# Kernel tuning notes

Hardware: AMD Instinct MI355X
Metric: run time of the kernel (lower is better)

## Reference

```python
import jax, jax.numpy as jnp
import numpy as np
import math

EMBED = 1024
HEADS = 16
HEAD_DIM = EMBED // HEADS


def setup_inputs() -> dict:
    key = jax.random.key(0)
    ks = jax.random.split(key, 9)
    B, S = 2, 2048
    query = jax.random.normal(ks[0], (B, S, EMBED), dtype=jnp.float32)
    key_t = jax.random.normal(ks[1], (B, S, EMBED), dtype=jnp.float32)
    value = jax.random.normal(ks[2], (B, S, EMBED), dtype=jnp.float32)
    mask = jax.random.randint(ks[3], (B, 1, S, S), 0, 2, dtype=jnp.int32)
    # nn.Linear(head_dim, head_dim, bias=False) weights: [out, in]
    sc = 1.0 / math.sqrt(HEAD_DIM)
    Wq = jax.random.uniform(ks[4], (HEAD_DIM, HEAD_DIM), jnp.float32, -sc, sc)
    Wk = jax.random.uniform(ks[5], (HEAD_DIM, HEAD_DIM), jnp.float32, -sc, sc)
    Wv = jax.random.uniform(ks[6], (HEAD_DIM, HEAD_DIM), jnp.float32, -sc, sc)
    so = 1.0 / math.sqrt(EMBED)
    Wo = jax.random.uniform(ks[7], (EMBED, EMBED), jnp.float32, -so, so)
    bo = jax.random.uniform(ks[8], (EMBED,), jnp.float32, -so, so)
    return {"query": query, "key": key_t, "value": value, "mask": mask,
            "Wq": Wq, "Wk": Wk, "Wv": Wv, "Wo": Wo, "bo": bo}


def reference(query, key, value, mask, Wq, Wk, Wv, Wo, bo):
    B, Sq, E = query.shape
    Sk = key.shape[1]
    H, D = HEADS, HEAD_DIM
    # Faithful raw reshape into heads (as in the torch source, no transpose)
    q = query.reshape(B, H, Sq, D)
    k = key.reshape(B, H, Sk, D)
    v = value.reshape(B, H, Sk, D)
    # per-head_dim Linear (bias-free): x @ W.T
    Q = jnp.einsum('bhsd,ed->bhse', q, Wq)
    K = jnp.einsum('bhsd,ed->bhse', k, Wk)
    V = jnp.einsum('bhsd,ed->bhse', v, Wv)
    scores = jnp.einsum('bhqd,bhkd->bhqk', Q, K)  # [B,H,Sq,Sk]
    scores = jnp.where(mask == 0, jnp.float32(-1e20), scores)
    # NOTE: source divides by sqrt(embed_size), not sqrt(head_dim)
    attn = jax.nn.softmax(scores / jnp.float32(math.sqrt(E)), axis=-1)
    out = jnp.einsum('bhqk,bhkd->bhqd', attn, V).reshape(B, Sq, H * D)
    return out @ Wo.T + bo
```

## Files before the change

### kernel.cpp

```cpp
#include <hip/hip_runtime.h>

typedef __attribute__((ext_vector_type(8))) short short8;
typedef __attribute__((ext_vector_type(4))) float f32x4;
typedef __attribute__((ext_vector_type(2))) int int2v;
typedef __attribute__((ext_vector_type(4))) int int4v;

__device__ __forceinline__ short f2bf(float f) {
  unsigned u = __builtin_bit_cast(unsigned, f);
  u += 0x7fff + ((u >> 16) & 1);
  return (short)(u >> 16);
}

__device__ __forceinline__ int pk2bf(float lo, float hi) {
#if defined(__gfx950__) && __has_builtin(__builtin_amdgcn_cvt_pk_bf16_f32)
  typedef __attribute__((ext_vector_type(2))) __bf16 bf16x2;
  bf16x2 v = __builtin_amdgcn_cvt_pk_bf16_f32(lo, hi);
  return __builtin_bit_cast(int, v);
#else
  return (int)(unsigned short)(short)f2bf(lo) | (((int)f2bf(hi)) << 16);
#endif
}

__device__ __forceinline__ short8 pack8(f32x4 a, f32x4 b) {
  int4v t;
  t.x = pk2bf(a[0], a[1]);
  t.y = pk2bf(a[2], a[3]);
  t.z = pk2bf(b[0], b[1]);
  t.w = pk2bf(b[2], b[3]);
  return __builtin_bit_cast(short8, t);
}

__device__ __forceinline__ float fand(float p, int m) {
  return __builtin_bit_cast(float, __builtin_bit_cast(int, p) & m);
}

__device__ __forceinline__ float fexp2(float x) {
#if __has_builtin(__builtin_amdgcn_exp2f)
  return __builtin_amdgcn_exp2f(x);
#else
  return exp2f(x);
#endif
}

__device__ __forceinline__ float bf2f(short s) {
  return __builtin_bit_cast(float, ((int)(unsigned short)s) << 16);
}

__device__ __forceinline__ void glds16(const short* g, short* lbase, int lane) {
#if __has_builtin(__builtin_amdgcn_global_load_lds)
  __builtin_amdgcn_global_load_lds(
      (const __attribute__((address_space(1))) unsigned int*)g,
      (__attribute__((address_space(3))) unsigned int*)lbase, 16, 0, 0);
#else
  *(short8*)(lbase + lane * 8) = *(const short8*)g;
#endif
}

__global__ __launch_bounds__(256) void prep(const float* __restrict__ q,
                                            const float* __restrict__ k,
                                            const float* __restrict__ v,
                                            const float* __restrict__ Wq,
                                            const float* __restrict__ Wk,
                                            const float* __restrict__ Wv,
                                            const float* __restrict__ Wo,
                                            const int* __restrict__ mask,
                                            short* __restrict__ Qp,
                                            short* __restrict__ Kp,
                                            short* __restrict__ Vtp,
                                            short* __restrict__ Wob,
                                            unsigned* __restrict__ mmod) {
  const int bid = blockIdx.x;
  const int tid = threadIdx.x;

  if (bid >= 4096) {
    const int mb = bid - 4096;
    const int ka = mb & 31, bq = mb >> 5;
    const int b_ = bq >> 4, qb = bq & 15;
    const int wv = tid >> 6, qd = (tid >> 4) & 3, m16_ = tid & 15;
    const int* mbase = mask + b_ * 4194304 + (qb * 128 + wv * 32) * 2048 + ka * 64 + m16_;
    unsigned d = 0;
#pragma unroll
    for (int p = 0; p < 8; ++p) {
      const int* mr = mbase + ((p >> 2) * 16 + qd * 4 + (p & 3)) * 2048;
#pragma unroll
      for (int bb = 0; bb < 4; ++bb)
        if (mr[bb * 16] != 0) d |= 1u << (p * 4 + bb);
    }
    mmod[mb * 256 + tid] = d;
    return;
  }
  if (bid >= 3072) {
    const int i = ((bid - 3072) * 256 + tid) * 4;
    const f32x4 x = *(const f32x4*)&Wo[i];
    int2v o;
    o.x = pk2bf(x[0], x[1]);
    o.y = pk2bf(x[2], x[3]);
    *(int2v*)&Wob[i] = o;
    return;
  }

  __shared__ short xt[64][72];
  __shared__ short ot[64][72];
  const int mode = bid >> 10;
  const int bt = bid & 1023;
  const float* X;
  const float* W;
  float scale;
  if (mode == 0) { X = q; W = Wq; scale = 0.045084220f; }
  else if (mode == 1) { X = k; W = Wk; scale = 1.0f; }
  else { X = v; W = Wv; scale = 1.0f; }

  const int r0 = bt * 64;
  const int row = tid >> 2, seg = (tid & 3) * 16;
  const f32x4* xs = (const f32x4*)(X + (r0 + row) * 64 + seg);
  const f32x4 x0 = xs[0], x1 = xs[1], x2 = xs[2], x3 = xs[3];
  *(short8*)&xt[row][seg] = pack8(x0, x1);
  *(short8*)&xt[row][seg + 8] = pack8(x2, x3);
  __syncthreads();

  const int lane = tid & 63, wave = tid >> 6;
  const int m16 = lane & 15, quad = lane >> 4;

  const short8 a0 = *(const short8*)&xt[wave * 16 + m16][quad * 8];
  const short8 a1 = *(const short8*)&xt[wave * 16 + m16][32 + quad * 8];

  f32x4 acc[4];
#pragma unroll
  for (int nt = 0; nt < 4; ++nt) {
    const f32x4* wp0 = (const f32x4*)&W[(nt * 16 + m16) * 64 + quad * 8];
    const f32x4* wp1 = (const f32x4*)&W[(nt * 16 + m16) * 64 + 32 + quad * 8];
    const short8 b0 = pack8(wp0[0], wp0[1]);
    const short8 b1 = pack8(wp1[0], wp1[1]);
    f32x4 z = (f32x4){0.f, 0.f, 0.f, 0.f};
    z = __builtin_amdgcn_mfma_f32_16x16x32_bf16(a0, b0, z, 0, 0, 0);
    z = __builtin_amdgcn_mfma_f32_16x16x32_bf16(a1, b1, z, 0, 0, 0);
    acc[nt] = z;
  }

  if (mode != 2) {
#pragma unroll
    for (int nt = 0; nt < 4; ++nt)
#pragma unroll
      for (int r = 0; r < 4; ++r)
        ot[wave * 16 + quad * 4 + r][nt * 16 + m16] = f2bf(acc[nt][r] * scale);
  } else {
#pragma unroll
    for (int nt = 0; nt < 4; ++nt)
#pragma unroll
      for (int r = 0; r < 4; ++r)
        ot[nt * 16 + m16][16 * quad + 4 * r + wave] = f2bf(acc[nt][r]);
  }
  __syncthreads();

  const int orow = tid >> 2, opart = tid & 3;
  if (mode != 2) {
    short* dst = (mode == 0 ? Qp : Kp) + (r0 + orow) * 64 + opart * 16;
    *(short8*)&dst[0] = *(const short8*)&ot[orow][opart * 16];
    *(short8*)&dst[8] = *(const short8*)&ot[orow][opart * 16 + 8];
  } else {
    const int bh = r0 >> 11, s0 = r0 & 2047;
    short* dst = Vtp + bh * 131072 + orow * 2048 + s0 + opart * 16;
    *(short8*)&dst[0] = *(const short8*)&ot[orow][opart * 16];
    *(short8*)&dst[8] = *(const short8*)&ot[orow][opart * 16 + 8];
  }
}

__global__ __launch_bounds__(256) void flashs(const short* __restrict__ Qp,
                                              const short* __restrict__ Kp,
                                              const short* __restrict__ Vt,
                                              const unsigned* __restrict__ mmod,
                                              short* __restrict__ Opart,
                                              float* __restrict__ lpart) {
  __shared__ __attribute__((aligned(16))) short kt[2][4096];
  __shared__ __attribute__((aligned(16))) short vt[2][4096];
  __shared__ __attribute__((aligned(16))) short pt[128][72];
  const int tid = threadIdx.x;
  const int bid = blockIdx.x;
  const int local = bid >> 3;
  const int khalf = local & 1;
  const int qblk = (local >> 1) & 15;
  const int bh = (bid & 7) * 4 + (local >> 5);
  const int q0 = qblk << 7;
  const int b = bh >> 4;
  const short* Qh = Qp + bh * 131072;
  const short* Kh = Kp + bh * 131072;
  const short* Vh = Vt + bh * 131072;
  const int lane = tid & 63, wave = tid >> 6;
  const int m16 = lane & 15, quad = lane >> 4;
  const int srow = lane >> 3, sj = (lane & 7) ^ srow;
  const int msh = m16 * 4;
  const int koff = m16 * 128 + ((quad ^ (m16 & 7)) * 16);
  const unsigned* mqb = mmod + (b * 16 + qblk) * 32 * 256 + tid;

  short8 aq[2][2];
#pragma unroll
  for (int g = 0; g < 2; ++g)
#pragma unroll
    for (int h = 0; h < 2; ++h)
      aq[g][h] = *(const short8*)&Qh[(q0 + wave * 32 + g * 16 + m16) * 64 + h * 32 + quad * 8];

  float l[2][4];
  f32x4 oacc[2][4];
#pragma unroll
  for (int g = 0; g < 2; ++g)
#pragma unroll
    for (int r = 0; r < 4; ++r) l[g][r] = 0.f;
#pragma unroll
  for (int g = 0; g < 2; ++g)
#pragma unroll
    for (int dt = 0; dt < 4; ++dt) oacc[g][dt] = (f32x4){0.f, 0.f, 0.f, 0.f};

  const int kaEnd = khalf * 16 + 15;

  auto stage = [&](int buf, int ka) {
#pragma unroll
    for (int t = 0; t < 2; ++t) {
      const int crow = wave * 16 + t * 8;
      glds16(Kh + (ka * 64 + crow + srow) * 64 + sj * 8, &kt[buf][crow * 64], lane);
      glds16(Vh + (crow + srow) * 2048 + ka * 64 + sj * 8, &vt[buf][crow * 64], lane);
    }
  };

  auto body = [&](int ka, int buf, unsigned mwU, unsigned& mwN) {
    __syncthreads();
    if (ka < kaEnd) {
      stage(buf ^ 1, ka + 1);
      mwN = mqb[(ka + 1) * 256];
    }

    f32x4 s[2][4];
#pragma unroll
    for (int nt = 0; nt < 4; ++nt) {
      const int o0 = nt * 2048 + koff;
      const short8 kb0 = *(const short8*)((const char*)&kt[buf][0] + o0);
      const short8 kb1 = *(const short8*)((const char*)&kt[buf][0] + (o0 ^ 64));
#pragma unroll
      for (int g = 0; g < 2; ++g) {
        f32x4 z = (f32x4){0.f, 0.f, 0.f, 0.f};
        z = __builtin_amdgcn_mfma_f32_16x16x32_bf16(aq[g][0], kb0, z, 0, 0, 0);
        z = __builtin_amdgcn_mfma_f32_16x16x32_bf16(aq[g][1], kb1, z, 0, 0, 0);
        s[g][nt] = z;
      }
    }

#pragma unroll
    for (int g = 0; g < 2; ++g) {
#pragma unroll
      for (int r = 0; r < 4; ++r) {
        const int pb = (g * 4 + r) * 4;
        float p[4];
#pragma unroll
        for (int nt = 0; nt < 4; ++nt) {
          const int m = ((int)(mwU << (31 - (pb + nt)))) >> 31;
          p[nt] = fand(fexp2(s[g][nt][r]), m);
        }
        l[g][r] += (p[0] + p[1]) + (p[2] + p[3]);
        int2v pp;
        pp.x = pk2bf(p[0], p[1]);
        pp.y = pk2bf(p[2], p[3]);
        *(int2v*)&pt[wave * 32 + g * 16 + quad * 4 + r][msh] = pp;
      }
    }

    short8 ap[2][2];
#pragma unroll
    for (int g = 0; g < 2; ++g)
#pragma unroll
      for (int h = 0; h < 2; ++h)
        ap[g][h] = *(const short8*)&pt[wave * 32 + g * 16 + m16][h * 32 + quad * 8];

#pragma unroll
    for (int dt = 0; dt < 4; ++dt) {
      const int o0 = dt * 2048 + koff;
      const short8 vb0 = *(const short8*)((const char*)&vt[buf][0] + o0);
      const short8 vb1 = *(const short8*)((const char*)&vt[buf][0] + (o0 ^ 64));
#pragma unroll
      for (int g = 0; g < 2; ++g) {
        f32x4 z = oacc[g][dt];
        z = __builtin_amdgcn_mfma_f32_16x16x32_bf16(ap[g][0], vb0, z, 0, 0, 0);
        z = __builtin_amdgcn_mfma_f32_16x16x32_bf16(ap[g][1], vb1, z, 0, 0, 0);
        oacc[g][dt] = z;
      }
    }
  };

  unsigned mwA, mwB = 0;
  const int ka0 = khalf * 16;
  stage(0, ka0);
  mwA = mqb[ka0 * 256];

  for (int kk = 0; kk < 8; ++kk) {
    body(ka0 + 2 * kk, 0, mwA, mwB);
    body(ka0 + 2 * kk + 1, 1, mwB, mwA);
  }

  short* Oh = Opart + khalf * 4194304;
  float* lh = lpart + khalf * 65536;
#pragma unroll
  for (int g = 0; g < 2; ++g)
#pragma unroll
    for (int r = 0; r < 4; ++r) {
#pragma unroll
      for (int off = 1; off < 16; off <<= 1) l[g][r] += __shfl_xor(l[g][r], off, 16);
      const float inv = 1.0f / l[g][r];
#pragma unroll
      for (int dt = 0; dt < 4; ++dt)
        pt[wave * 32 + g * 16 + quad * 4 + r][dt * 16 + m16] = f2bf(oacc[g][dt][r] * inv);
      if (m16 == 0) lh[bh * 2048 + q0 + wave * 32 + g * 16 + quad * 4 + r] = l[g][r];
    }

  const int orow = lane >> 1, opart = lane & 1;
  const int prow = wave * 32 + orow;
  short* og = Oh + (bh * 2048 + q0 + prow) * 64 + opart * 32;
#pragma unroll
  for (int c = 0; c < 32; c += 8)
    *(short8*)&og[c] = *(const short8*)&pt[prow][opart * 32 + c];
}

__global__ __launch_bounds__(256) void combineO(const short* __restrict__ O0,
                                                const short* __restrict__ O1,
                                                const float* __restrict__ lp,
                                                short* __restrict__ Ob) {
  const int gid = blockIdx.x * 256 + threadIdx.x;
  const int e0 = gid * 8;
  const int row = e0 >> 6;
  const float l1 = lp[row], l2 = lp[65536 + row];
  const float is = 1.0f / (l1 + l2);
  const float w1 = l1 * is, w2 = l2 * is;
  const short8 a = *(const short8*)&O0[e0];
  const short8 c = *(const short8*)&O1[e0];
  float f[8];
#pragma unroll
  for (int j = 0; j < 8; ++j) f[j] = w1 * bf2f(a[j]) + w2 * bf2f(c[j]);
  int4v o;
  o.x = pk2bf(f[0], f[1]);
  o.y = pk2bf(f[2], f[3]);
  o.z = pk2bf(f[4], f[5]);
  o.w = pk2bf(f[6], f[7]);
  *(short8*)&Ob[e0] = __builtin_bit_cast(short8, o);
}

__global__ __launch_bounds__(256) void outproj(const short* __restrict__ Ob,
                                               const short* __restrict__ Wob,
                                               const float* __restrict__ bo,
                                               float* __restrict__ out) {
  __shared__ short at[64][72];
  __shared__ short bt[128][72];
  const int tid = threadIdx.x;
  const int bid = blockIdx.x;
  const int ct = bid >> 6, rt = bid & 63;
  const int r0 = rt * 64, c0 = ct * 128;
  const int lane = tid & 63, wave = tid >> 6;
  const int mr = (wave >> 1) * 32, nc = (wave & 1) * 64;
  const int m16 = lane & 15, quad = lane >> 4;
  const int arow = tid >> 2, apart = tid & 3;
  const int brow = tid >> 1, bhalf = (tid & 1) * 32;

  f32x4 acc[2][4];
#pragma unroll
  for (int mt = 0; mt < 2; ++mt)
#pragma unroll
    for (int nt = 0; nt < 4; ++nt) acc[mt][nt] = (f32x4){0.f, 0.f, 0.f, 0.f};

  for (int kc = 0; kc < 16; ++kc) {
    __syncthreads();
    const short* ag = &Ob[(r0 + arow) * 1024 + kc * 64 + apart * 16];
    const short* bg = &Wob[(c0 + brow) * 1024 + kc * 64 + bhalf];
    *(short8*)&at[arow][apart * 16] = *(const short8*)&ag[0];
    *(short8*)&at[arow][apart * 16 + 8] = *(const short8*)&ag[8];
    *(short8*)&bt[brow][bhalf] = *(const short8*)&bg[0];
    *(short8*)&bt[brow][bhalf + 8] = *(const short8*)&bg[8];
    *(short8*)&bt[brow][bhalf + 16] = *(const short8*)&bg[16];
    *(short8*)&bt[brow][bhalf + 24] = *(const short8*)&bg[24];
    __syncthreads();

#pragma unroll
    for (int kh = 0; kh < 2; ++kh) {
      short8 af[2], bf[4];
#pragma unroll
      for (int i = 0; i < 2; ++i)
        af[i] = *(const short8*)&at[mr + i * 16 + m16][kh * 32 + quad * 8];
#pragma unroll
      for (int j = 0; j < 4; ++j)
        bf[j] = *(const short8*)&bt[nc + j * 16 + m16][kh * 32 + quad * 8];
#pragma unroll
      for (int mt = 0; mt < 2; ++mt)
#pragma unroll
        for (int nt = 0; nt < 4; ++nt)
          acc[mt][nt] = __builtin_amdgcn_mfma_f32_16x16x32_bf16(af[mt], bf[nt], acc[mt][nt], 0, 0, 0);
    }
  }

#pragma unroll
  for (int nt = 0; nt < 4; ++nt) {
    const int col = c0 + nc + nt * 16 + m16;
    const float bias = bo[col];
#pragma unroll
    for (int mt = 0; mt < 2; ++mt)
#pragma unroll
      for (int rr = 0; rr < 4; ++rr)
        out[(r0 + mr + mt * 16 + quad * 4 + rr) * 1024 + col] = acc[mt][nt][rr] + bias;
  }
}

extern "C" void kernel_launch(void* const* d_in, const int* in_sizes, int n_in,
                              void* d_out, int out_size, void* d_ws, size_t ws_size,
                              hipStream_t stream) {
  const float* query = (const float*)d_in[0];
  const float* key = (const float*)d_in[1];
  const float* value = (const float*)d_in[2];
  const int* mask = (const int*)d_in[3];
  const float* Wq = (const float*)d_in[4];
  const float* Wk = (const float*)d_in[5];
  const float* Wv = (const float*)d_in[6];
  const float* Wo = (const float*)d_in[7];
  const float* bo = (const float*)d_in[8];
  float* out = (float*)d_out;

  char* ws = (char*)d_ws;
  short* Qp = (short*)(ws);
  short* Kp = (short*)(ws + 8388608);
  short* Vt = (short*)(ws + 16777216);
  short* Opart = (short*)(ws + 25165824);
  short* Wob = (short*)(ws + 41943040);
  float* lp = (float*)(ws + 44040192);
  unsigned* mmod = (unsigned*)(ws + 44564480);
  short* Ob = Qp;

  prep<<<5120, 256, 0, stream>>>(query, key, value, Wq, Wk, Wv, Wo, mask,
                                 Qp, Kp, Vt, Wob, mmod);
  flashs<<<1024, 256, 0, stream>>>(Qp, Kp, Vt, mmod, Opart, lp);
  combineO<<<2048, 256, 0, stream>>>(Opart, Opart + 4194304, lp, Ob);
  outproj<<<512, 256, 0, stream>>>(Ob, Wob, bo, out);
}
```

Baseline: 246.3 us.

## Drop LDS staging in flash kernel, shrink q-tile, fuse split-K combine into outproj

The attention kernel now reads K and V fragments straight from global memory instead of double-buffering them through LDS with async loads. It uses 64-query tiles (one 16-row group per wave), doubling the grid to 2048 blocks, and declares occupancy 4 in launch bounds. The mask bit layout is regenerated to match the new tile shape. The combineO kernel is removed: the output projection now merges the two key-half partial outputs with their l weights while loading its A tile, which saves one launch and an intermediate buffer round trip. The trade is more global/L2 traffic for K/V, which is no longer reused across waves through LDS, in exchange for fewer syncs and higher occupancy.

```diff
diff --git a/kernel.cpp b/kernel.cpp
--- a/kernel.cpp
+++ b/kernel.cpp
@@ -44,16 +44,6 @@
 
 __device__ __forceinline__ float bf2f(short s) {
   return __builtin_bit_cast(float, ((int)(unsigned short)s) << 16);
-}
-
-__device__ __forceinline__ void glds16(const short* g, short* lbase, int lane) {
-#if __has_builtin(__builtin_amdgcn_global_load_lds)
-  __builtin_amdgcn_global_load_lds(
-      (const __attribute__((address_space(1))) unsigned int*)g,
-      (__attribute__((address_space(3))) unsigned int*)lbase, 16, 0, 0);
-#else
-  *(short8*)(lbase + lane * 8) = *(const short8*)g;
-#endif
 }
 
 __global__ __launch_bounds__(256) void prep(const float* __restrict__ q,
@@ -74,17 +64,21 @@
 
   if (bid >= 4096) {
     const int mb = bid - 4096;
-    const int ka = mb & 31, bq = mb >> 5;
-    const int b_ = bq >> 4, qb = bq & 15;
+    const int kp = mb & 15, bq = mb >> 4;
+    const int b_ = bq >> 5, q64 = bq & 31;
     const int wv = tid >> 6, qd = (tid >> 4) & 3, m16_ = tid & 15;
-    const int* mbase = mask + b_ * 4194304 + (qb * 128 + wv * 32) * 2048 + ka * 64 + m16_;
     unsigned d = 0;
 #pragma unroll
-    for (int p = 0; p < 8; ++p) {
-      const int* mr = mbase + ((p >> 2) * 16 + qd * 4 + (p & 3)) * 2048;
-#pragma unroll
-      for (int bb = 0; bb < 4; ++bb)
-        if (mr[bb * 16] != 0) d |= 1u << (p * 4 + bb);
+    for (int hb = 0; hb < 2; ++hb) {
+      const int ka = kp * 2 + hb;
+#pragma unroll
+      for (int r = 0; r < 4; ++r) {
+        const int* mr = mask + b_ * 4194304 +
+                        (q64 * 64 + wv * 16 + qd * 4 + r) * 2048 + ka * 64 + m16_;
+#pragma unroll
+        for (int nt = 0; nt < 4; ++nt)
+          if (mr[nt * 16] != 0) d |= 1u << (hb * 16 + r * 4 + nt);
+      }
     }
     mmod[mb * 256 + tid] = d;
     return;
@@ -165,182 +159,114 @@
   }
 }
 
-__global__ __launch_bounds__(256) void flashs(const short* __restrict__ Qp,
-                                              const short* __restrict__ Kp,
-                                              const short* __restrict__ Vt,
-                                              const unsigned* __restrict__ mmod,
-                                              short* __restrict__ Opart,
-                                              float* __restrict__ lpart) {
-  __shared__ __attribute__((aligned(16))) short kt[2][4096];
-  __shared__ __attribute__((aligned(16))) short vt[2][4096];
-  __shared__ __attribute__((aligned(16))) short pt[128][72];
+__global__ __launch_bounds__(256, 4) void flashc(const short* __restrict__ Qp,
+                                                 const short* __restrict__ Kp,
+                                                 const short* __restrict__ Vt,
+                                                 const unsigned* __restrict__ mmod,
+                                                 short* __restrict__ Opart,
+                                                 float* __restrict__ lpart) {
+  __shared__ __attribute__((aligned(16))) short pt[64][72];
   const int tid = threadIdx.x;
   const int bid = blockIdx.x;
   const int local = bid >> 3;
   const int khalf = local & 1;
-  const int qblk = (local >> 1) & 15;
-  const int bh = (bid & 7) * 4 + (local >> 5);
-  const int q0 = qblk << 7;
+  const int qblk = (local >> 1) & 31;
+  const int bh = (bid & 7) * 4 + (local >> 6);
+  const int q0 = qblk << 6;
   const int b = bh >> 4;
   const short* Qh = Qp + bh * 131072;
   const short* Kh = Kp + bh * 131072;
   const short* Vh = Vt + bh * 131072;
   const int lane = tid & 63, wave = tid >> 6;
   const int m16 = lane & 15, quad = lane >> 4;
-  const int srow = lane >> 3, sj = (lane & 7) ^ srow;
   const int msh = m16 * 4;
-  const int koff = m16 * 128 + ((quad ^ (m16 & 7)) * 16);
-  const unsigned* mqb = mmod + (b * 16 + qblk) * 32 * 256 + tid;
-
-  short8 aq[2][2];
-#pragma unroll
-  for (int g = 0; g < 2; ++g)
-#pragma unroll
-    for (int h = 0; h < 2; ++h)
-      aq[g][h] = *(const short8*)&Qh[(q0 + wave * 32 + g * 16 + m16) * 64 + h * 32 + quad * 8];
-
-  float l[2][4];
-  f32x4 oacc[2][4];
-#pragma unroll
-  for (int g = 0; g < 2; ++g)
-#pragma unroll
-    for (int r = 0; r < 4; ++r) l[g][r] = 0.f;
-#pragma unroll
-  for (int g = 0; g < 2; ++g)
-#pragma unroll
-    for (int dt = 0; dt < 4; ++dt) oacc[g][dt] = (f32x4){0.f, 0.f, 0.f, 0.f};
-
-  const int kaEnd = khalf * 16 + 15;
-
-  auto stage = [&](int buf, int ka) {
-#pragma unroll
-    for (int t = 0; t < 2; ++t) {
-      const int crow = wave * 16 + t * 8;
-      glds16(Kh + (ka * 64 + crow + srow) * 64 + sj * 8, &kt[buf][crow * 64], lane);
-      glds16(Vh + (crow + srow) * 2048 + ka * 64 + sj * 8, &vt[buf][crow * 64], lane);
+  const unsigned* mq = mmod + ((b * 32 + qblk) * 16) * 256 + tid;
+
+  short8 aq[2];
+#pragma unroll
+  for (int h = 0; h < 2; ++h)
+    aq[h] = *(const short8*)&Qh[(q0 + wave * 16 + m16) * 64 + h * 32 + quad * 8];
+
+  float l[4] = {0.f, 0.f, 0.f, 0.f};
+  f32x4 oacc[4];
+#pragma unroll
+  for (int dt = 0; dt < 4; ++dt) oacc[dt] = (f32x4){0.f, 0.f, 0.f, 0.f};
+
+  auto body = [&](int ka, unsigned mw, int bitbase) {
+    const int k0 = ka << 6;
+
+    f32x4 s[4];
+#pragma unroll
+    for (int nt = 0; nt < 4; ++nt) {
+      const short* kr = &Kh[(k0 + nt * 16 + m16) * 64 + quad * 8];
+      const short8 kb0 = *(const short8*)&kr[0];
+      const short8 kb1 = *(const short8*)&kr[32];
+      f32x4 z = (f32x4){0.f, 0.f, 0.f, 0.f};
+      z = __builtin_amdgcn_mfma_f32_16x16x32_bf16(aq[0], kb0, z, 0, 0, 0);
+      z = __builtin_amdgcn_mfma_f32_16x16x32_bf16(aq[1], kb1, z, 0, 0, 0);
+      s[nt] = z;
+    }
+
+#pragma unroll
+    for (int r = 0; r < 4; ++r) {
+      float p[4];
+#pragma unroll
+      for (int nt = 0; nt < 4; ++nt) {
+        const int sh = 31 - (bitbase + r * 4 + nt);
+        const int m = ((int)(mw << sh)) >> 31;
+        p[nt] = fand(fexp2(s[nt][r]), m);
+      }
+      l[r] += (p[0] + p[1]) + (p[2] + p[3]);
+      int2v pp;
+      pp.x = pk2bf(p[0], p[1]);
+      pp.y = pk2bf(p[2], p[3]);
+      *(int2v*)&pt[wave * 16 + quad * 4 + r][msh] = pp;
+    }
+
+    const short8 ap0 = *(const short8*)&pt[wave * 16 + m16][quad * 8];
+    const short8 ap1 = *(const short8*)&pt[wave * 16 + m16][32 + quad * 8];
+#pragma unroll
+    for (int dt = 0; dt < 4; ++dt) {
+      const short* vr = &Vh[(dt * 16 + m16) * 2048 + k0 + quad * 8];
+      const short8 vb0 = *(const short8*)&vr[0];
+      const short8 vb1 = *(const short8*)&vr[32];
+      f32x4 z = oacc[dt];
+      z = __builtin_amdgcn_mfma_f32_16x16x32_bf16(ap0, vb0, z, 0, 0, 0);
+      z = __builtin_amdgcn_mfma_f32_16x16x32_bf16(ap1, vb1, z, 0, 0, 0);
+      oacc[dt] = z;
     }
   };
 
-  auto body = [&](int ka, int buf, unsigned mwU, unsigned& mwN) {
-    __syncthreads();
-    if (ka < kaEnd) {
-      stage(buf ^ 1, ka + 1);
-      mwN = mqb[(ka + 1) * 256];
-    }
-
-    f32x4 s[2][4];
-#pragma unroll
-    for (int nt = 0; nt < 4; ++nt) {
-      const int o0 = nt * 2048 + koff;
-      const short8 kb0 = *(const short8*)((const char*)&kt[buf][0] + o0);
-      const short8 kb1 = *(const short8*)((const char*)&kt[buf][0] + (o0 ^ 64));
-#pragma unroll
-      for (int g = 0; g < 2; ++g) {
-        f32x4 z = (f32x4){0.f, 0.f, 0.f, 0.f};
-        z = __builtin_amdgcn_mfma_f32_16x16x32_bf16(aq[g][0], kb0, z, 0, 0, 0);
-        z = __builtin_amdgcn_mfma_f32_16x16x32_bf16(aq[g][1], kb1, z, 0, 0, 0);
-        s[g][nt] = z;
-      }
-    }
-
-#pragma unroll
-    for (int g = 0; g < 2; ++g) {
-#pragma unroll
-      for (int r = 0; r < 4; ++r) {
-        const int pb = (g * 4 + r) * 4;
-        float p[4];
-#pragma unroll
-        for (int nt = 0; nt < 4; ++nt) {
-          const int m = ((int)(mwU << (31 - (pb + nt)))) >> 31;
-          p[nt] = fand(fexp2(s[g][nt][r]), m);
-        }
-        l[g][r] += (p[0] + p[1]) + (p[2] + p[3]);
-        int2v pp;
-        pp.x = pk2bf(p[0], p[1]);
-        pp.y = pk2bf(p[2], p[3]);
-        *(int2v*)&pt[wave * 32 + g * 16 + quad * 4 + r][msh] = pp;
-      }
-    }
-
-    short8 ap[2][2];
-#pragma unroll
-    for (int g = 0; g < 2; ++g)
-#pragma unroll
-      for (int h = 0; h < 2; ++h)
-        ap[g][h] = *(const short8*)&pt[wave * 32 + g * 16 + m16][h * 32 + quad * 8];
-
-#pragma unroll
-    for (int dt = 0; dt < 4; ++dt) {
-      const int o0 = dt * 2048 + koff;
-      const short8 vb0 = *(const short8*)((const char*)&vt[buf][0] + o0);
-      const short8 vb1 = *(const short8*)((const char*)&vt[buf][0] + (o0 ^ 64));
-#pragma unroll
-      for (int g = 0; g < 2; ++g) {
-        f32x4 z = oacc[g][dt];
-        z = __builtin_amdgcn_mfma_f32_16x16x32_bf16(ap[g][0], vb0, z, 0, 0, 0);
-        z = __builtin_amdgcn_mfma_f32_16x16x32_bf16(ap[g][1], vb1, z, 0, 0, 0);
-        oacc[g][dt] = z;
-      }
-    }
-  };
-
-  unsigned mwA, mwB = 0;
   const int ka0 = khalf * 16;
-  stage(0, ka0);
-  mwA = mqb[ka0 * 256];
-
   for (int kk = 0; kk < 8; ++kk) {
-    body(ka0 + 2 * kk, 0, mwA, mwB);
-    body(ka0 + 2 * kk + 1, 1, mwB, mwA);
+    const unsigned mw = mq[(khalf * 8 + kk) * 256];
+    body(ka0 + 2 * kk, mw, 0);
+    body(ka0 + 2 * kk + 1, mw, 16);
   }
 
   short* Oh = Opart + khalf * 4194304;
   float* lh = lpart + khalf * 65536;
 #pragma unroll
-  for (int g = 0; g < 2; ++g)
-#pragma unroll
-    for (int r = 0; r < 4; ++r) {
-#pragma unroll
-      for (int off = 1; off < 16; off <<= 1) l[g][r] += __shfl_xor(l[g][r], off, 16);
-      const float inv = 1.0f / l[g][r];
-#pragma unroll
-      for (int dt = 0; dt < 4; ++dt)
-        pt[wave * 32 + g * 16 + quad * 4 + r][dt * 16 + m16] = f2bf(oacc[g][dt][r] * inv);
-      if (m16 == 0) lh[bh * 2048 + q0 + wave * 32 + g * 16 + quad * 4 + r] = l[g][r];
-    }
-
-  const int orow = lane >> 1, opart = lane & 1;
-  const int prow = wave * 32 + orow;
-  short* og = Oh + (bh * 2048 + q0 + prow) * 64 + opart * 32;
-#pragma unroll
-  for (int c = 0; c < 32; c += 8)
-    *(short8*)&og[c] = *(const short8*)&pt[prow][opart * 32 + c];
-}
-
-__global__ __launch_bounds__(256) void combineO(const short* __restrict__ O0,
-                                                const short* __restrict__ O1,
-                                                const float* __restrict__ lp,
-                                                short* __restrict__ Ob) {
-  const int gid = blockIdx.x * 256 + threadIdx.x;
-  const int e0 = gid * 8;
-  const int row = e0 >> 6;
-  const float l1 = lp[row], l2 = lp[65536 + row];
-  const float is = 1.0f / (l1 + l2);
-  const float w1 = l1 * is, w2 = l2 * is;
-  const short8 a = *(const short8*)&O0[e0];
-  const short8 c = *(const short8*)&O1[e0];
-  float f[8];
-#pragma unroll
-  for (int j = 0; j < 8; ++j) f[j] = w1 * bf2f(a[j]) + w2 * bf2f(c[j]);
-  int4v o;
-  o.x = pk2bf(f[0], f[1]);
-  o.y = pk2bf(f[2], f[3]);
-  o.z = pk2bf(f[4], f[5]);
-  o.w = pk2bf(f[6], f[7]);
-  *(short8*)&Ob[e0] = __builtin_bit_cast(short8, o);
-}
-
-__global__ __launch_bounds__(256) void outproj(const short* __restrict__ Ob,
+  for (int r = 0; r < 4; ++r) {
+#pragma unroll
+    for (int off = 1; off < 16; off <<= 1) l[r] += __shfl_xor(l[r], off, 16);
+    const float inv = 1.0f / l[r];
+#pragma unroll
+    for (int dt = 0; dt < 4; ++dt)
+      pt[wave * 16 + quad * 4 + r][dt * 16 + m16] = f2bf(oacc[dt][r] * inv);
+    if (m16 == 0) lh[bh * 2048 + q0 + wave * 16 + quad * 4 + r] = l[r];
+  }
+
+  const int orow = lane >> 2, opart = lane & 3;
+  const int prow = wave * 16 + orow;
+  short* og = Oh + (bh * 2048 + q0 + prow) * 64 + opart * 16;
+  *(short8*)&og[0] = *(const short8*)&pt[prow][opart * 16];
+  *(short8*)&og[8] = *(const short8*)&pt[prow][opart * 16 + 8];
+}
+
+__global__ __launch_bounds__(256) void outproj(const short* __restrict__ O0,
+                                               const short* __restrict__ O1,
+                                               const float* __restrict__ lp,
                                                const short* __restrict__ Wob,
                                                const float* __restrict__ bo,
                                                float* __restrict__ out) {
@@ -355,6 +281,8 @@
   const int m16 = lane & 15, quad = lane >> 4;
   const int arow = tid >> 2, apart = tid & 3;
   const int brow = tid >> 1, bhalf = (tid & 1) * 32;
+  const int rr = r0 + arow;
+  const int lbase = (rr >> 7) * 2048 + (rr & 127) * 16;
 
   f32x4 acc[2][4];
 #pragma unroll
@@ -363,11 +291,27 @@
     for (int nt = 0; nt < 4; ++nt) acc[mt][nt] = (f32x4){0.f, 0.f, 0.f, 0.f};
 
   for (int kc = 0; kc < 16; ++kc) {
+    const float l1 = lp[lbase + kc], l2 = lp[65536 + lbase + kc];
+    const float is = 1.0f / (l1 + l2);
+    const float w1 = l1 * is, w2 = l2 * is;
+    const short8 a0 = *(const short8*)&O0[rr * 1024 + kc * 64 + apart * 16];
+    const short8 a1 = *(const short8*)&O1[rr * 1024 + kc * 64 + apart * 16];
+    const short8 a0b = *(const short8*)&O0[rr * 1024 + kc * 64 + apart * 16 + 8];
+    const short8 a1b = *(const short8*)&O1[rr * 1024 + kc * 64 + apart * 16 + 8];
+    const short* bg = &Wob[(c0 + brow) * 1024 + kc * 64 + bhalf];
     __syncthreads();
-    const short* ag = &Ob[(r0 + arow) * 1024 + kc * 64 + apart * 16];
-    const short* bg = &Wob[(c0 + brow) * 1024 + kc * 64 + bhalf];
-    *(short8*)&at[arow][apart * 16] = *(const short8*)&ag[0];
-    *(short8*)&at[arow][apart * 16 + 8] = *(const short8*)&ag[8];
+    int4v ca, cb;
+    float f[8];
+#pragma unroll
+    for (int j = 0; j < 8; ++j) f[j] = w1 * bf2f(a0[j]) + w2 * bf2f(a1[j]);
+    ca.x = pk2bf(f[0], f[1]); ca.y = pk2bf(f[2], f[3]);
+    ca.z = pk2bf(f[4], f[5]); ca.w = pk2bf(f[6], f[7]);
+#pragma unroll
+    for (int j = 0; j < 8; ++j) f[j] = w1 * bf2f(a0b[j]) + w2 * bf2f(a1b[j]);
+    cb.x = pk2bf(f[0], f[1]); cb.y = pk2bf(f[2], f[3]);
+    cb.z = pk2bf(f[4], f[5]); cb.w = pk2bf(f[6], f[7]);
+    *(short8*)&at[arow][apart * 16] = __builtin_bit_cast(short8, ca);
+    *(short8*)&at[arow][apart * 16 + 8] = __builtin_bit_cast(short8, cb);
     *(short8*)&bt[brow][bhalf] = *(const short8*)&bg[0];
     *(short8*)&bt[brow][bhalf + 8] = *(const short8*)&bg[8];
     *(short8*)&bt[brow][bhalf + 16] = *(const short8*)&bg[16];
@@ -398,8 +342,8 @@
 #pragma unroll
     for (int mt = 0; mt < 2; ++mt)
 #pragma unroll
-      for (int rr = 0; rr < 4; ++rr)
-        out[(r0 + mr + mt * 16 + quad * 4 + rr) * 1024 + col] = acc[mt][nt][rr] + bias;
+      for (int rr2 = 0; rr2 < 4; ++rr2)
+        out[(r0 + mr + mt * 16 + quad * 4 + rr2) * 1024 + col] = acc[mt][nt][rr2] + bias;
   }
 }
 
@@ -425,11 +369,9 @@
   short* Wob = (short*)(ws + 41943040);
   float* lp = (float*)(ws + 44040192);
   unsigned* mmod = (unsigned*)(ws + 44564480);
-  short* Ob = Qp;
 
   prep<<<5120, 256, 0, stream>>>(query, key, value, Wq, Wk, Wv, Wo, mask,
                                  Qp, Kp, Vt, Wob, mmod);
-  flashs<<<1024, 256, 0, stream>>>(Qp, Kp, Vt, mmod, Opart, lp);
-  combineO<<<2048, 256, 0, stream>>>(Opart, Opart + 4194304, lp, Ob);
-  outproj<<<512, 256, 0, stream>>>(Ob, Wob, bo, out);
-}
+  flashc<<<2048, 256, 0, stream>>>(Qp, Kp, Vt, mmod, Opart, lp);
+  outproj<<<512, 256, 0, stream>>>(Opart, Opart + 4194304, lp, Wob, bo, out);
+}
```

After: 408.6 us. +65.9%, slower.
